# Kernel tuning notes

Measured on AMD Instinct MI355X. Metric: run time of the kernel, lower is better.

Reference implementation:

```python
import jax, jax.numpy as jnp
import numpy as np

B, C, H, W = 4, 192, 128, 128
GAMMA = 0.9
HIDDEN = int(C * 2.66)  # 510
EPS_NORM = 1e-12
EPS_LN = 1e-5


def conv2d(x, w, b, groups=1, pad=0):
    # x: (B,Cin,H,W), w: (Cout, Cin//groups, kh, kw)
    y = jax.lax.conv_general_dilated(
        x, w, window_strides=(1, 1), padding=[(pad, pad), (pad, pad)],
        dimension_numbers=("NCHW", "OIHW", "NCHW"), feature_group_count=groups)
    return y + b[None, :, None, None]


def setup_inputs() -> dict:
    key = jax.random.key(0)
    ks = jax.random.split(key, 32)
    s = 0.02
    d = {
        "Q": jax.random.normal(ks[0], (B, C, H, W), jnp.float32),
        "Fn": jax.random.normal(ks[1], (B, C, H, W), jnp.float32),
        "temperature": jnp.ones((1,), jnp.float32),
        # q/k/v projections: 1x1 conv then depthwise 3x3
        "qw1": jax.random.normal(ks[2], (C, C, 1, 1)) * s, "qb1": jnp.zeros((C,)),
        "qw2": jax.random.normal(ks[3], (C, 1, 3, 3)) * s, "qb2": jnp.zeros((C,)),
        "kw1": jax.random.normal(ks[4], (C, C, 1, 1)) * s, "kb1": jnp.zeros((C,)),
        "kw2": jax.random.normal(ks[5], (C, 1, 3, 3)) * s, "kb2": jnp.zeros((C,)),
        "vw1": jax.random.normal(ks[6], (C, C, 1, 1)) * s, "vb1": jnp.zeros((C,)),
        "vw2": jax.random.normal(ks[7], (C, 1, 3, 3)) * s, "vb2": jnp.zeros((C,)),
        "ow": jax.random.normal(ks[8], (C, C, 1, 1)) * s, "ob": jnp.zeros((C,)),
        # LayerNorm over channels
        "ln_w": jnp.ones((C,)), "ln_b": jnp.zeros((C,)),
        # FFN: proj_in 1x1 -> 2*HIDDEN, dw 3x3 (groups=2*HIDDEN), proj_out HIDDEN -> C
        "fi_w": jax.random.normal(ks[9], (2 * HIDDEN, C, 1, 1)) * s, "fi_b": jnp.zeros((2 * HIDDEN,)),
        "fd_w": jax.random.normal(ks[10], (2 * HIDDEN, 1, 3, 3)) * s, "fd_b": jnp.zeros((2 * HIDDEN,)),
        "fo_w": jax.random.normal(ks[11], (C, HIDDEN, 1, 1)) * s, "fo_b": jnp.zeros((C,)),
    }
    return {k: v.astype(jnp.float32) for k, v in d.items()}


def _forward(Q, Fn, temperature, qw1, qb1, qw2, qb2, kw1, kb1, kw2, kb2,
             vw1, vb1, vw2, vb2, ow, ob, ln_w, ln_b, fi_w, fi_b, fd_w, fd_b, fo_w, fo_b):
    q = conv2d(conv2d(Q, qw1, qb1), qw2, qb2, groups=C, pad=1).reshape(B, C, H * W)
    k = conv2d(conv2d(Fn, kw1, kb1), kw2, kb2, groups=C, pad=1).reshape(B, C, H * W)
    v = conv2d(conv2d(Fn, vw1, vb1), vw2, vb2, groups=C, pad=1).reshape(B, C, H * W)
    # L2 normalize along spatial (last) dim
    q = q / jnp.maximum(jnp.linalg.norm(q, axis=-1, keepdims=True), EPS_NORM)
    k = k / jnp.maximum(jnp.linalg.norm(k, axis=-1, keepdims=True), EPS_NORM)
    attn = jnp.einsum("bcn,bdn->bcd", q, k) * temperature  # (B,C,C)
    attn = jax.nn.softmax(attn, axis=-1)
    k_keep = max(1, int(C * GAMMA))
    topk_vals, _ = jax.lax.top_k(attn, k_keep)
    threshold = topk_vals[:, :, -1:]
    attn = attn * (attn >= threshold).astype(attn.dtype)
    out = jnp.einsum("bcd,bdn->bcn", attn, v).reshape(B, C, H, W)
    Fa = conv2d(out, ow, ob)
    # LayerNorm over channel dim (per pixel)
    xp = Fa.transpose(0, 2, 3, 1)  # (B,H,W,C)
    mu = xp.mean(-1, keepdims=True)
    var = ((xp - mu) ** 2).mean(-1, keepdims=True)
    xn = ((xp - mu) / jnp.sqrt(var + EPS_LN)) * ln_w + ln_b
    xn = xn.transpose(0, 3, 1, 2)
    # FFN
    h = conv2d(xn, fi_w, fi_b)
    h = conv2d(h, fd_w, fd_b, groups=2 * HIDDEN, pad=1)
    x1, x2 = h[:, :HIDDEN], h[:, HIDDEN:]
    h = x1 * jax.nn.gelu(x2, approximate=False)
    ffn_out = conv2d(h, fo_w, fo_b)
    return Fa + ffn_out


def reference(Q, Fn, temperature, qw1, qb1, qw2, qb2, kw1, kb1, kw2, kb2,
              vw1, vb1, vw2, vb2, ow, ob, ln_w, ln_b, fi_w, fi_b, fd_w, fd_b, fo_w, fo_b):
    return _forward(Q, Fn, temperature, qw1, qb1, qw2, qb2, kw1, kb1, kw2, kb2,
                    vw1, vb1, vw2, vb2, ow, ob, ln_w, ln_b, fi_w, fi_b, fd_w, fd_b, fo_w, fo_b)
```

## Files before the change

### kernel.cpp

```cpp
#include <hip/hip_runtime.h>
#include <math.h>
#include <float.h>

#define NPIX 16384
#define CC 192
#define BB 4
#define HHH 128
#define WWW 128
#define HID 510
#define HID2 1020
#define KKEEP 172
#define KSPLIT 16

typedef unsigned short ushort;
typedef unsigned int uint32;
using f32x4  = __attribute__((ext_vector_type(4))) float;
using bf16x8 = __attribute__((ext_vector_type(8))) short;

__device__ __forceinline__ float bf2f(ushort u) {
  union { float f; unsigned int i; } x; x.i = ((unsigned int)u) << 16; return x.f;
}
__device__ __forceinline__ ushort f2bf(float f) {
  union { float f; unsigned int i; } x; x.f = f;
  unsigned int r = (x.i + 0x7FFFu + ((x.i >> 16) & 1u)) >> 16;
// ... 3 lines not shown
struct __align__(16) us8 { ushort u[8]; };
struct __align__(8)  us4 { ushort u[4]; };

__global__ __launch_bounds__(256) void k_wconv(
    const float* __restrict__ fiw, const float* __restrict__ fow,
    ushort* __restrict__ fiwb, ushort* __restrict__ fowb)
{
  const int idx = blockIdx.x * 256 + threadIdx.x;
  if (idx < 1024 * 192) {
    const int r = idx / 192, c = idx % 192;
    fiwb[idx] = (r < HID2) ? f2bf(fiw[r * 192 + c]) : (ushort)0;
  }
  const int i2 = idx - 1024 * 192;
  if (i2 >= 0 && i2 < 192 * 512) {
    const int r = i2 / 512, c = i2 % 512;
    fowb[i2] = (c < HID) ? f2bf(fow[r * HID + c]) : (ushort)0;
  }
}

__global__ __launch_bounds__(256) void k_tsplit(
    const float* __restrict__ X, ushort* __restrict__ Xh, ushort* __restrict__ Xl)
{
  __shared__ float ld[64][261];
  const int b = blockIdx.z;
  const int c0 = blockIdx.y * 64;
  const int px0 = blockIdx.x * 256;
  const int tid = threadIdx.x;
  #pragma unroll
  for (int i = 0; i < 16; ++i) {
    const int u = i * 256 + tid;
    const int r = u >> 6, p4 = (u & 63) * 4;
    const float4 v = *reinterpret_cast<const float4*>(
        X + ((size_t)b * CC + c0 + r) * NPIX + px0 + p4);
    ld[r][p4] = v.x; ld[r][p4 + 1] = v.y; ld[r][p4 + 2] = v.z; ld[r][p4 + 3] = v.w;
  }
  __syncthreads();
  const int c8 = (tid & 7) * 8;
  #pragma unroll
  for (int it = 0; it < 8; ++it) {
    const int pl = it * 32 + (tid >> 3);
    us8 hi, lo;
    #pragma unroll
    for (int j = 0; j < 8; ++j) {
      const float v = ld[c8 + j][pl];
      const ushort h = f2bf(v);
      hi.u[j] = h; lo.u[j] = f2bf(v - bf2f(h));
    }
    const size_t off = ((size_t)b * NPIX + px0 + pl) * CC + c0 + c8;
    *reinterpret_cast<us8*>(Xh + off) = hi;
    *reinterpret_cast<us8*>(Xl + off) = lo;
  }
}

__global__ __launch_bounds__(512) void k_nt3res(
    const float* __restrict__ W,
    const ushort* __restrict__ Bh, const ushort* __restrict__ Bl,
    const float* __restrict__ bias, float* __restrict__ C,
    long long sAb)
{
  __shared__ ushort As[2][64][200];
  __shared__ ushort Bs[2][128][200];
  const int b = blockIdx.z;
  const int n0 = blockIdx.x * 128;
  const int m0 = blockIdx.y * 64;
  const int tid = threadIdx.x;
  const int lane = tid & 63;
  const int wave = tid >> 6;
  const int wm = wave >> 2, wn = wave & 3;
  const float*  Wb  = W  + (size_t)b * sAb;
  const ushort* Bhb = Bh + (size_t)b * NPIX * CC;
  const ushort* Blb = Bl + (size_t)b * NPIX * CC;

  #pragma unroll
  for (int i = 0; i < 6; ++i) {
    const int u = i * 512 + tid;
    const int r = u / 48, c = (u % 48) * 4;
    const float4 v = *reinterpret_cast<const float4*>(Wb + (size_t)(m0 + r) * CC + c);
    const float e[4] = {v.x, v.y, v.z, v.w};
    us4 hi, lo;
    #pragma unroll
    for (int t = 0; t < 4; ++t) {
      const ushort h = f2bf(e[t]);
      hi.u[t] = h; lo.u[t] = f2bf(e[t] - bf2f(h));
    }
    *reinterpret_cast<us4*>(&As[0][r][c]) = hi;
    *reinterpret_cast<us4*>(&As[1][r][c]) = lo;
  }
  #pragma unroll
  for (int i = 0; i < 6; ++i) {
    const int u = i * 512 + tid;
    const int r = u / 24, c = (u % 24) * 8;
    *reinterpret_cast<us8*>(&Bs[0][r][c]) =
        *reinterpret_cast<const us8*>(Bhb + (size_t)(n0 + r) * CC + c);
    *reinterpret_cast<us8*>(&Bs[1][r][c]) =
        *reinterpret_cast<const us8*>(Blb + (size_t)(n0 + r) * CC + c);
  }
  __syncthreads();

  f32x4 acc[2][2];
  #pragma unroll
  for (int i = 0; i < 2; ++i)
    #pragma unroll
    for (int j = 0; j < 2; ++j) acc[i][j] = (f32x4){0.f, 0.f, 0.f, 0.f};

  #pragma unroll
  for (int kk = 0; kk < 6; ++kk) {
    bf16x8 af[2][2], bfg[2][2];
    #pragma unroll
    for (int mi = 0; mi < 2; ++mi)
      #pragma unroll
      for (int p = 0; p < 2; ++p)
        af[mi][p] = *reinterpret_cast<const bf16x8*>(
            &As[p][wm * 32 + mi * 16 + (lane & 15)][kk * 32 + (lane >> 4) * 8]);
    #pragma unroll
    for (int ni = 0; ni < 2; ++ni)
      #pragma unroll
      for (int p = 0; p < 2; ++p)
        bfg[ni][p] = *reinterpret_cast<const bf16x8*>(
            &Bs[p][wn * 32 + ni * 16 + (lane & 15)][kk * 32 + (lane >> 4) * 8]);
    #pragma unroll
    for (int mi = 0; mi < 2; ++mi)
      #pragma unroll
      for (int ni = 0; ni < 2; ++ni) {
        acc[mi][ni] = __builtin_amdgcn_mfma_f32_16x16x32_bf16(
            af[mi][0], bfg[ni][0], acc[mi][ni], 0, 0, 0);
        acc[mi][ni] = __builtin_amdgcn_mfma_f32_16x16x32_bf16(
            af[mi][0], bfg[ni][1], acc[mi][ni], 0, 0, 0);
        acc[mi][ni] = __builtin_amdgcn_mfma_f32_16x16x32_bf16(
            af[mi][1], bfg[ni][0], acc[mi][ni], 0, 0, 0);
      }
  }

  #pragma unroll
  for (int mi = 0; mi < 2; ++mi)
    #pragma unroll
    for (int r = 0; r < 4; ++r) {
      const int m = m0 + wm * 32 + mi * 16 + (lane >> 4) * 4 + r;
      const float bv = bias[m];
      #pragma unroll
      for (int ni = 0; ni < 2; ++ni) {
        const int n = n0 + wn * 32 + ni * 16 + (lane & 15);
        C[(size_t)b * CC * NPIX + (size_t)m * NPIX + n] = acc[mi][ni][r] + bv;
      }
    }
}

__global__ __launch_bounds__(512) void k_nt3res2(
    const float* __restrict__ W1, const float* __restrict__ W2,
    const ushort* __restrict__ Bh, const ushort* __restrict__ Bl,
    const float* __restrict__ b1, const float* __restrict__ b2,
    float* __restrict__ C1, float* __restrict__ C2)
{
  __shared__ ushort As[2][64][200];
  __shared__ ushort Bs[2][128][200];
  const int b = blockIdx.z;
  const int n0 = blockIdx.x * 128;
  const bool sel = blockIdx.y >= 3;
  const int m0 = (sel ? (blockIdx.y - 3) : blockIdx.y) * 64;
  const float* W = sel ? W2 : W1;
  const float* bias = sel ? b2 : b1;
  float* C = sel ? C2 : C1;
  const int tid = threadIdx.x;
  const int lane = tid & 63;
  const int wave = tid >> 6;
  const int wm = wave >> 2, wn = wave & 3;
  const ushort* Bhb = Bh + (size_t)b * NPIX * CC;
  const ushort* Blb = Bl + (size_t)b * NPIX * CC;

  #pragma unroll
  for (int i = 0; i < 6; ++i) {
    const int u = i * 512 + tid;
    const int r = u / 48, c = (u % 48) * 4;
    const float4 v = *reinterpret_cast<const float4*>(W + (size_t)(m0 + r) * CC + c);
    const float e[4] = {v.x, v.y, v.z, v.w};
    us4 hi, lo;
    #pragma unroll
    for (int t = 0; t < 4; ++t) {
      const ushort h = f2bf(e[t]);
      hi.u[t] = h; lo.u[t] = f2bf(e[t] - bf2f(h));
    }
    *reinterpret_cast<us4*>(&As[0][r][c]) = hi;
    *reinterpret_cast<us4*>(&As[1][r][c]) = lo;
  }
  #pragma unroll
  for (int i = 0; i < 6; ++i) {
    const int u = i * 512 + tid;
    const int r = u / 24, c = (u % 24) * 8;
    *reinterpret_cast<us8*>(&Bs[0][r][c]) =
        *reinterpret_cast<const us8*>(Bhb + (size_t)(n0 + r) * CC + c);
    *reinterpret_cast<us8*>(&Bs[1][r][c]) =
        *reinterpret_cast<const us8*>(Blb + (size_t)(n0 + r) * CC + c);
  }
  __syncthreads();

  f32x4 acc[2][2];
  #pragma unroll
  for (int i = 0; i < 2; ++i)
    #pragma unroll
    for (int j = 0; j < 2; ++j) acc[i][j] = (f32x4){0.f, 0.f, 0.f, 0.f};

  #pragma unroll
  for (int kk = 0; kk < 6; ++kk) {
    bf16x8 af[2][2], bfg[2][2];
    #pragma unroll
    for (int mi = 0; mi < 2; ++mi)
      #pragma unroll
      for (int p = 0; p < 2; ++p)
        af[mi][p] = *reinterpret_cast<const bf16x8*>(
            &As[p][wm * 32 + mi * 16 + (lane & 15)][kk * 32 + (lane >> 4) * 8]);
    #pragma unroll
    for (int ni = 0; ni < 2; ++ni)
      #pragma unroll
      for (int p = 0; p < 2; ++p)
        bfg[ni][p] = *reinterpret_cast<const bf16x8*>(
            &Bs[p][wn * 32 + ni * 16 + (lane & 15)][kk * 32 + (lane >> 4) * 8]);
    #pragma unroll
    for (int mi = 0; mi < 2; ++mi)
      #pragma unroll
      for (int ni = 0; ni < 2; ++ni) {
        acc[mi][ni] = __builtin_amdgcn_mfma_f32_16x16x32_bf16(
            af[mi][0], bfg[ni][0], acc[mi][ni], 0, 0, 0);
        acc[mi][ni] = __builtin_amdgcn_mfma_f32_16x16x32_bf16(
            af[mi][0], bfg[ni][1], acc[mi][ni], 0, 0, 0);
        acc[mi][ni] = __builtin_amdgcn_mfma_f32_16x16x32_bf16(
            af[mi][1], bfg[ni][0], acc[mi][ni], 0, 0, 0);
      }
  }

  #pragma unroll
  for (int mi = 0; mi < 2; ++mi)
    #pragma unroll
    for (int r = 0; r < 4; ++r) {
      const int m = m0 + wm * 32 + mi * 16 + (lane >> 4) * 4 + r;
      const float bv = bias[m];
      #pragma unroll
      for (int ni = 0; ni < 2; ++ni) {
        const int n = n0 + wn * 32 + ni * 16 + (lane & 15);
        C[(size_t)b * CC * NPIX + (size_t)m * NPIX + n] = acc[mi][ni][r] + bv;
      }
    }
}

__global__ __launch_bounds__(256) void k_fi(
    const ushort* __restrict__ Aw, const ushort* __restrict__ Bt,
    const float* __restrict__ bias, ushort* __restrict__ H)
{
  __shared__ ushort lds[64 * 200 + 128 * 200];
  ushort (*As)[200] = reinterpret_cast<ushort(*)[200]>(lds);
  ushort (*Bs)[200] = reinterpret_cast<ushort(*)[200]>(lds + 64 * 200);
  ushort (*Cs)[132] = reinterpret_cast<ushort(*)[132]>(lds);
  const int z = blockIdx.z;
  const int n0 = blockIdx.x * 128;
  const int m0 = blockIdx.y * 64;
  const int tid = threadIdx.x;
  const int lane = tid & 63;
  const int wave = tid >> 6;
  const int wm = wave >> 1, wn = wave & 1;
  const ushort* Bb = Bt + (size_t)z * NPIX * CC;
  ushort* Hb = H + (size_t)z * 1024 * NPIX;

  #pragma unroll
  for (int i = 0; i < 6; ++i) {
    const int u = i * 256 + tid;
    const int r = u / 24, c = (u % 24) * 8;
    *reinterpret_cast<us8*>(&As[r][c]) =
        *reinterpret_cast<const us8*>(Aw + (size_t)(m0 + r) * CC + c);
  }
  #pragma unroll
  for (int i = 0; i < 12; ++i) {
    const int u = i * 256 + tid;
    const int r = u / 24, c = (u % 24) * 8;
    *reinterpret_cast<us8*>(&Bs[r][c]) =
        *reinterpret_cast<const us8*>(Bb + (size_t)(n0 + r) * CC + c);
  }
  __syncthreads();

  f32x4 acc[2][4];
  #pragma unroll
  for (int i = 0; i < 2; ++i)
    #pragma unroll
    for (int j = 0; j < 4; ++j) acc[i][j] = (f32x4){0.f, 0.f, 0.f, 0.f};

  #pragma unroll
  for (int kk = 0; kk < 6; ++kk) {
    bf16x8 af[2], bfg[4];
    #pragma unroll
    for (int mi = 0; mi < 2; ++mi)
      af[mi] = *reinterpret_cast<const bf16x8*>(
          &As[wm * 32 + mi * 16 + (lane & 15)][kk * 32 + (lane >> 4) * 8]);
    #pragma unroll
    for (int ni = 0; ni < 4; ++ni)
      bfg[ni] = *reinterpret_cast<const bf16x8*>(
          &Bs[wn * 64 + ni * 16 + (lane & 15)][kk * 32 + (lane >> 4) * 8]);
    #pragma unroll
    for (int mi = 0; mi < 2; ++mi)
      #pragma unroll
      for (int ni = 0; ni < 4; ++ni)
        acc[mi][ni] = __builtin_amdgcn_mfma_f32_16x16x32_bf16(
            af[mi], bfg[ni], acc[mi][ni], 0, 0, 0);
  }

  __syncthreads();
  #pragma unroll
  for (int mi = 0; mi < 2; ++mi)
    #pragma unroll
    for (int rr = 0; rr < 4; ++rr) {
      const int rloc = wm * 32 + mi * 16 + (lane >> 4) * 4 + rr;
      const int m = m0 + rloc;
      const float bv = (m < HID2) ? bias[m] : 0.f;
      #pragma unroll
      for (int ni = 0; ni < 4; ++ni) {
        const int cc = wn * 64 + ni * 16 + (lane & 15);
        Cs[rloc][cc] = f2bf(acc[mi][ni][rr] + bv);
      }
    }
  __syncthreads();
  #pragma unroll
  for (int it = 0; it < 4; ++it) {
    const int r = it * 16 + (tid >> 4);
    const int c8 = (tid & 15) * 8;
    *reinterpret_cast<us8*>(Hb + (size_t)(m0 + r) * NPIX + n0 + c8) =
        *reinterpret_cast<const us8*>(&Cs[r][c8]);
  }
}

__global__ __launch_bounds__(256) void k_fo(
    const ushort* __restrict__ Aw, const ushort* __restrict__ Bt,
    const float* __restrict__ bias, const float* __restrict__ res,
    float* __restrict__ C)
{
  __shared__ ushort As[64][520];
  __shared__ ushort Bs[2][128][136];
  const int z = blockIdx.z;
  const int n0 = blockIdx.x * 128;
  const int m0 = blockIdx.y * 64;
  const int tid = threadIdx.x;
  const int lane = tid & 63;
  const int wave = tid >> 6;
  const int wm = wave >> 1, wn = wave & 1;
  const ushort* Bb = Bt + (size_t)z * NPIX * 512;
  const float* resb = res + (size_t)z * CC * NPIX;
  float* Cb = C + (size_t)z * CC * NPIX;

  #pragma unroll
  for (int i = 0; i < 16; ++i) {
    const int u = i * 256 + tid;
    const int r = u >> 6, c = (u & 63) * 8;
    *reinterpret_cast<us8*>(&As[r][c]) =
        *reinterpret_cast<const us8*>(Aw + (size_t)(m0 + r) * 512 + c);
  }
  #pragma unroll
  for (int i = 0; i < 8; ++i) {
    const int u = i * 256 + tid;
    const int r = u >> 4, c = (u & 15) * 8;
    *reinterpret_cast<us8*>(&Bs[0][r][c]) =
        *reinterpret_cast<const us8*>(Bb + (size_t)(n0 + r) * 512 + c);
  }
  __syncthreads();

  f32x4 acc[2][4];
  #pragma unroll
  for (int i = 0; i < 2; ++i)
    #pragma unroll
    for (int j = 0; j < 4; ++j) acc[i][j] = (f32x4){0.f, 0.f, 0.f, 0.f};

  for (int t = 0; t < 4; ++t) {
    us8 rg[8];
    if (t < 3) {
      #pragma unroll
      for (int i = 0; i < 8; ++i) {
        const int u = i * 256 + tid;
        const int r = u >> 4, c = (u & 15) * 8;
        rg[i] = *reinterpret_cast<const us8*>(
            Bb + (size_t)(n0 + r) * 512 + (t + 1) * 128 + c);
      }
    }
    const int cur = t & 1;
    #pragma unroll
    for (int ks = 0; ks < 4; ++ks) {
      bf16x8 af[2], bfg[4];
      #pragma unroll
      for (int mi = 0; mi < 2; ++mi)
        af[mi] = *reinterpret_cast<const bf16x8*>(
            &As[wm * 32 + mi * 16 + (lane & 15)][t * 128 + ks * 32 + (lane >> 4) * 8]);
      #pragma unroll
      for (int ni = 0; ni < 4; ++ni)
        bfg[ni] = *reinterpret_cast<const bf16x8*>(
            &Bs[cur][wn * 64 + ni * 16 + (lane & 15)][ks * 32 + (lane >> 4) * 8]);
      #pragma unroll
      for (int mi = 0; mi < 2; ++mi)
        #pragma unroll
        for (int ni = 0; ni < 4; ++ni)
          acc[mi][ni] = __builtin_amdgcn_mfma_f32_16x16x32_bf16(
              af[mi], bfg[ni], acc[mi][ni], 0, 0, 0);
    }
    if (t < 3) {
      #pragma unroll
      for (int i = 0; i < 8; ++i) {
        const int u = i * 256 + tid;
        const int r = u >> 4, c = (u & 15) * 8;
        *reinterpret_cast<us8*>(&Bs[cur ^ 1][r][c]) = rg[i];
      }
    }
    __syncthreads();
  }

  #pragma unroll
  for (int mi = 0; mi < 2; ++mi)
    #pragma unroll
    for (int r = 0; r < 4; ++r) {
      const int m = m0 + wm * 32 + mi * 16 + (lane >> 4) * 4 + r;
      const float bv = bias[m];
      #pragma unroll
      for (int ni = 0; ni < 4; ++ni) {
        const int n = n0 + wn * 64 + ni * 16 + (lane & 15);
        Cb[(size_t)m * NPIX + n] = acc[mi][ni][r] + bv + resb[(size_t)m * NPIX + n];
      }
    }
}

__global__ __launch_bounds__(256) void k_attn_mfma(
    const ushort* __restrict__ qh, const ushort* __restrict__ ql,
    const ushort* __restrict__ kh, const ushort* __restrict__ kl,
    float* __restrict__ part)
{
  __shared__ ushort As[2][64][40];
  __shared__ ushort Bs[2][64][40];
  const int b = blockIdx.z;
  const int tr = blockIdx.x / 3, tc = blockIdx.x % 3;
  const int r0 = tr * 64, c0 = tc * 64;
  const int k0 = blockIdx.y * (NPIX / KSPLIT);
  const int tid = threadIdx.x;
  const int lane = tid & 63;
  const int wave = tid >> 6;
  const int wm = wave >> 1, wn = wave & 1;

  f32x4 acc[2][2];
  #pragma unroll
  for (int i = 0; i < 2; ++i)
    #pragma unroll
    for (int j = 0; j < 2; ++j) acc[i][j] = (f32x4){0.f, 0.f, 0.f, 0.f};

  const int ar = tid >> 2, ak = (tid & 3) * 8;

  for (int kc = 0; kc < NPIX / KSPLIT; kc += 32) {
    const size_t qo = (size_t)(b * CC + r0 + ar) * NPIX + k0 + kc + ak;
    const size_t ko = (size_t)(b * CC + c0 + ar) * NPIX + k0 + kc + ak;
// ... 16 lines not shown
        bfr[ni][p] = *reinterpret_cast<const bf16x8*>(
            &Bs[p][wn * 32 + ni * 16 + (lane & 15)][(lane >> 4) * 8]);
    #pragma unroll
    for (int mi = 0; mi < 2; ++mi)
      #pragma unroll
      for (int ni = 0; ni < 2; ++ni) {
        acc[mi][ni] = __builtin_amdgcn_mfma_f32_16x16x32_bf16(
            af[mi][0], bfr[ni][0], acc[mi][ni], 0, 0, 0);
        acc[mi][ni] = __builtin_amdgcn_mfma_f32_16x16x32_bf16(
            af[mi][0], bfr[ni][1], acc[mi][ni], 0, 0, 0);
        acc[mi][ni] = __builtin_amdgcn_mfma_f32_16x16x32_bf16(
            af[mi][1], bfr[ni][0], acc[mi][ni], 0, 0, 0);
      }
    __syncthreads();
  }

  float* pp = part + (size_t)(blockIdx.y * BB + b) * CC * CC;
  #pragma unroll
  for (int mi = 0; mi < 2; ++mi)
    #pragma unroll
    for (int r = 0; r < 4; ++r) {
      const int row = r0 + wm * 32 + mi * 16 + (lane >> 4) * 4 + r;
      #pragma unroll
      for (int ni = 0; ni < 2; ++ni) {
        const int col = c0 + wn * 32 + ni * 16 + (lane & 15);
        pp[(size_t)row * CC + col] = acc[mi][ni][r];
      }
    }
}

__device__ __forceinline__ void dw4(const float* __restrict__ Xc,
                                    const float* __restrict__ wt, float bv,
                                    int h, int w, float out[4])
{
  float a0, a1, a2, a3;
  a0 = a1 = a2 = a3 = bv;
  #pragma unroll
  for (int dy = 0; dy < 3; ++dy) {
    const int hh = h + dy - 1;
    if (hh < 0 || hh >= HHH) continue;
    const float* row = Xc + hh * WWW + w;
    const float xm = (w > 0) ? row[-1] : 0.f;
    const float4 xc = *reinterpret_cast<const float4*>(row);
    const float xp = (w < WWW - 4) ? row[4] : 0.f;
    const float w0 = wt[dy * 3 + 0], w1 = wt[dy * 3 + 1], w2 = wt[dy * 3 + 2];
    a0 += w0 * xm   + w1 * xc.x + w2 * xc.y;
    a1 += w0 * xc.x + w1 * xc.y + w2 * xc.z;
    a2 += w0 * xc.y + w1 * xc.z + w2 * xc.w;
    a3 += w0 * xc.z + w1 * xc.w + w2 * xp;
  }
  out[0] = a0; out[1] = a1; out[2] = a2; out[3] = a3;
}

__global__ __launch_bounds__(256) void k_dw3x3(
    const float* __restrict__ X, const float* __restrict__ W9,
    const float* __restrict__ bias, float* __restrict__ Y)
{
  const int b = blockIdx.z, c = blockIdx.y;
  const int p = blockIdx.x * 1024 + threadIdx.x * 4;
  const int h = p >> 7, w = p & 127;
  float o[4];
  dw4(X + (size_t)(b * CC + c) * NPIX, W9 + c * 9, bias[c], h, w, o);
  *reinterpret_cast<float4*>(Y + (size_t)(b * CC + c) * NPIX + p) =
      make_float4(o[0], o[1], o[2], o[3]);
}

__global__ __launch_bounds__(256) void k_dw3x3_split(
    const float* __restrict__ X, const float* __restrict__ W9,
    const float* __restrict__ bias, ushort* __restrict__ Yh,
    ushort* __restrict__ Yl)
{
  const int b = blockIdx.z, c = blockIdx.y;
  const int p = blockIdx.x * 1024 + threadIdx.x * 4;
  const int h = p >> 7, w = p & 127;
  float o[4];
  dw4(X + (size_t)(b * CC + c) * NPIX, W9 + c * 9, bias[c], h, w, o);
  us4 hi, lo;
  #pragma unroll
  for (int t = 0; t < 4; ++t) {
    const ushort hv = f2bf(o[t]);
    hi.u[t] = hv;
    lo.u[t] = f2bf(o[t] - bf2f(hv));
  }
  const size_t off = (size_t)(b * CC + c) * NPIX + p;
  *reinterpret_cast<us4*>(Yh + off) = hi;
  *reinterpret_cast<us4*>(Yl + off) = lo;
}

__global__ __launch_bounds__(256) void k_rownorm2(
    const ushort* __restrict__ qh, const ushort* __restrict__ ql,
    const ushort* __restrict__ kh, const ushort* __restrict__ kl,
    float* __restrict__ rq, float* __restrict__ rk)
{
  const int row = blockIdx.x;
  const ushort* H = blockIdx.y ? kh : qh;
  const ushort* L = blockIdx.y ? kl : ql;
  float* R = blockIdx.y ? rk : rq;
  const ushort* Hr = H + (size_t)row * NPIX;
  const ushort* Lr = L + (size_t)row * NPIX;
  float s = 0.f;
  for (int i = threadIdx.x * 8; i < NPIX; i += 2048) {
    const us8 a = *reinterpret_cast<const us8*>(Hr + i);
    const us8 bb = *reinterpret_cast<const us8*>(Lr + i);
    #pragma unroll
    for (int t = 0; t < 8; ++t) {
      const float v = bf2f(a.u[t]) + bf2f(bb.u[t]);
      s += v * v;
    }
  }
  __shared__ float sm[256];
  sm[threadIdx.x] = s; __syncthreads();
  for (int st = 128; st > 0; st >>= 1) {
    if (threadIdx.x < st) sm[threadIdx.x] += sm[threadIdx.x + st];
    __syncthreads();
  }
  if (threadIdx.x == 0) R[row] = 1.f / fmaxf(sqrtf(sm[0]), 1e-12f);
}

__global__ __launch_bounds__(192) void k_softmax_topk(
    const float* __restrict__ part, const float* __restrict__ rq,
    const float* __restrict__ rk, const float* __restrict__ temp,
    float* __restrict__ attnm)
{
  const int c = blockIdx.x, b = blockIdx.y, d = threadIdx.x;
  float s = 0.f;
  for (int ksp = 0; ksp < KSPLIT; ++ksp)
    s += part[(size_t)(ksp * BB + b) * CC * CC + c * CC + d];
  const float logit = s * rq[b * CC + c] * rk[b * CC + d] * temp[0];
  __shared__ float sa[CC], sb[CC];
  sa[d] = logit; __syncthreads();
  float mx = -FLT_MAX;
  for (int j = 0; j < CC; ++j) mx = fmaxf(mx, sa[j]);
  const float e = expf(logit - mx);
  sb[d] = e; __syncthreads();
  float sum = 0.f;
  for (int j = 0; j < CC; ++j) sum += sb[j];
  const float pv = e / sum;
  __syncthreads();
  sa[d] = pv; __syncthreads();
  int greater = 0;
  for (int j = 0; j < CC; ++j) greater += (sa[j] > pv) ? 1 : 0;
  const float cand = (greater < KKEEP) ? pv : FLT_MAX;
  sb[d] = cand; __syncthreads();
  float thr = FLT_MAX;
  for (int j = 0; j < CC; ++j) thr = fminf(thr, sb[j]);
  attnm[(size_t)(b * CC + c) * CC + d] = (pv >= thr) ? pv : 0.f;
}

__global__ __launch_bounds__(192) void k_mix(
    const float* __restrict__ ow, const float* __restrict__ attnm,
    float* __restrict__ M)
{
  const int c = blockIdx.x, b = blockIdx.y, d = threadIdx.x;
  float acc = 0.f;
  for (int e = 0; e < CC; ++e)
    acc += ow[c * CC + e] * attnm[(size_t)(b * CC + e) * CC + d];
  M[(size_t)(b * CC + c) * CC + d] = acc;
}

__global__ __launch_bounds__(256) void k_ln_t(
    const float* __restrict__ X, const float* __restrict__ lw,
    const float* __restrict__ lb, ushort* __restrict__ Y)
{
  const int b = blockIdx.y;
  const int n = blockIdx.x * 256 + threadIdx.x;
  const float* Xb = X + (size_t)b * CC * NPIX + n;
  float s = 0.f, s2 = 0.f;
  for (int ci = 0; ci < CC; ++ci) {
    const float v = Xb[(size_t)ci * NPIX];
// ... 104 lines not shown
    gsd[j * 129 + (px_l >> 1) + 1] = p1;
  }
  __syncthreads();

  const ushort* gsu = (const ushort*)gsd;
  const int px_l2 = tid;
  const int px = (h0 + (px_l2 >> 7)) * WWW + (px_l2 & 127);
  us8 v;
  #pragma unroll
  for (int t = 0; t < 8; ++t) v.u[t] = gsu[t * 258 + px_l2];
  *reinterpret_cast<us8*>(gt + ((size_t)z * NPIX + px) * 512 + c0) = v;
}

extern "C" void kernel_launch(void* const* d_in, const int* in_sizes, int n_in,
                              void* d_out, int out_size, void* d_ws, size_t ws_size,
                              hipStream_t stream)
{
  const float* Q    = (const float*)d_in[0];
  const float* Fn   = (const float*)d_in[1];
  const float* temp = (const float*)d_in[2];
  const float* qw1  = (const float*)d_in[3];
  const float* qb1  = (const float*)d_in[4];
  const float* qw2  = (const float*)d_in[5];
  const float* qb2  = (const float*)d_in[6];
  const float* kw1  = (const float*)d_in[7];
  const float* kb1  = (const float*)d_in[8];
  const float* kw2  = (const float*)d_in[9];
  const float* kb2  = (const float*)d_in[10];
  const float* vw1  = (const float*)d_in[11];
  const float* vb1  = (const float*)d_in[12];
  const float* vw2  = (const float*)d_in[13];
  const float* vb2  = (const float*)d_in[14];
  const float* ow   = (const float*)d_in[15];
  const float* ob   = (const float*)d_in[16];
  const float* lnw  = (const float*)d_in[17];
  const float* lnb  = (const float*)d_in[18];
  const float* fiw  = (const float*)d_in[19];
  const float* fib  = (const float*)d_in[20];
  const float* fdw  = (const float*)d_in[21];
  const float* fdb  = (const float*)d_in[22];
  const float* fow  = (const float*)d_in[23];
  const float* fob  = (const float*)d_in[24];
  float* out = (float*)d_out;

  char* ws = (char*)d_ws;
  const size_t P = 25165824UL;
  ushort* Qth = (ushort*)(ws + 0 * P);
  ushort* Qtl = (ushort*)(ws + 1 * P);
  ushort* Fth = (ushort*)(ws + 2 * P);
  ushort* Ftl = (ushort*)(ws + 3 * P);
  ushort* qh  = (ushort*)(ws + 4 * P);
  ushort* ql  = (ushort*)(ws + 5 * P);
  float*  vtmp = (float*)(ws + 0 * P);
  float*  vbuf = (float*)(ws + 2 * P);
  ushort* kh  = (ushort*)(ws + 0 * P);
  ushort* kl  = (ushort*)(ws + 1 * P);
  ushort* vth = (ushort*)(ws + 0 * P);
  ushort* vtl = (ushort*)(ws + 1 * P);
  char* smb = ws + 6 * P;
  float* rq    = (float*)(smb);
  float* rk    = (float*)(smb + 4096);
  float* part  = (float*)(smb + 8192);
  float* attnm = (float*)(smb + 8192 + 9437184);
  float* Mm    = (float*)(smb + 8192 + 9437184 + 589824);
  float*  Fa   = (float*)(ws + 4 * P);
  ushort* xnt  = (ushort*)(ws + 0 * P);
  ushort* h2   = (ushort*)(ws + 1 * P);
  ushort* gt2  = (ushort*)(ws + 6 * P);
  ushort* fiwb = (ushort*)(ws + 6 * P + 33554432UL);
  ushort* fowb = (ushort*)(ws + 6 * P + 33554432UL + 393216UL);
  float* bufT = out;

  dim3 blk(256);
  dim3 blk512(512);

  k_wconv<<<dim3(1152), blk, 0, stream>>>(fiw, fow, fiwb, fowb);
  k_tsplit<<<dim3(64, 3, BB), blk, 0, stream>>>(Q,  Qth, Qtl);
  k_tsplit<<<dim3(64, 3, BB), blk, 0, stream>>>(Fn, Fth, Ftl);
  k_nt3res<<<dim3(128, 3, BB), blk512, 0, stream>>>(qw1, Qth, Qtl, qb1, bufT, 0);
  k_dw3x3_split<<<dim3(16, CC, BB), blk, 0, stream>>>(bufT, qw2, qb2, qh, ql);
  k_nt3res2<<<dim3(128, 6, BB), blk512, 0, stream>>>(kw1, vw1, Fth, Ftl,
                                                     kb1, vb1, bufT, vtmp);
  k_dw3x3<<<dim3(16, CC, BB), blk, 0, stream>>>(vtmp, vw2, vb2, vbuf);
  k_dw3x3_split<<<dim3(16, CC, BB), blk, 0, stream>>>(bufT, kw2, kb2, kh, kl);
  k_rownorm2<<<dim3(BB * CC, 2), blk, 0, stream>>>(qh, ql, kh, kl, rq, rk);
  k_attn_mfma<<<dim3(9, KSPLIT, BB), blk, 0, stream>>>(qh, ql, kh, kl, part);
  k_softmax_topk<<<dim3(CC, BB), dim3(192), 0, stream>>>(part, rq, rk, temp, attnm);
  k_mix<<<dim3(CC, BB), dim3(192), 0, stream>>>(ow, attnm, Mm);
  k_tsplit<<<dim3(64, 3, BB), blk, 0, stream>>>(vbuf, vth, vtl);
  k_nt3res<<<dim3(128, 3, BB), blk512, 0, stream>>>(Mm, vth, vtl, ob, Fa,
                                                    (long long)CC * CC);
  k_ln_t<<<dim3(64, BB), blk, 0, stream>>>(Fa, lnw, lnb, xnt);
  for (int p = 0; p < 2; ++p) {
    const ushort* xn_p = xnt + (size_t)(2 * p) * NPIX * CC;
    const float*  fa_p = Fa + (size_t)(2 * p) * CC * NPIX;
    float* out_p = out + (size_t)(2 * p) * CC * NPIX;
    k_fi<<<dim3(128, 16, 2), blk, 0, stream>>>(fiwb, xn_p, fib, h2);
    k_dwglu3<<<dim3(64, 64, 2), blk, 0, stream>>>(h2, fdw, fdb, gt2);
    k_fo<<<dim3(128, 3, 2), blk, 0, stream>>>(fowb, gt2, fob, fa_p, out_p);
  }
}
```

Baseline: 628.3 us.

## Hold GEMM weight fragments in registers and stage hi/lo B halves sequentially

The 1x1-conv GEMM kernels now load weight (A) fragments straight from global memory into registers, with the bf16 hi/lo split done in registers, instead of staging them in LDS. The 3-term kernels also stage the B hi and lo halves one after the other through a single LDS buffer. This cuts LDS use per block, which should allow more blocks per CU, and removes LDS reads for A. In exchange it adds register pressure, an extra barrier phase, and uncoalesced per-lane weight loads.

```diff
diff --git a/kernel.cpp b/kernel.cpp
--- a/kernel.cpp
+++ b/kernel.cpp
@@ -79,14 +79,13 @@
   }
 }
 
-__global__ __launch_bounds__(512) void k_nt3res(
+__global__ __launch_bounds__(512) void k_nt3reg(
     const float* __restrict__ W,
     const ushort* __restrict__ Bh, const ushort* __restrict__ Bl,
     const float* __restrict__ bias, float* __restrict__ C,
     long long sAb)
 {
-  __shared__ ushort As[2][64][200];
-  __shared__ ushort Bs[2][128][200];
+  __shared__ ushort Bs[128][200];
   const int b = blockIdx.z;
   const int n0 = blockIdx.x * 128;
   const int m0 = blockIdx.y * 64;
@@ -98,64 +97,80 @@
   const ushort* Bhb = Bh + (size_t)b * NPIX * CC;
   const ushort* Blb = Bl + (size_t)b * NPIX * CC;
 
-  #pragma unroll
-  for (int i = 0; i < 6; ++i) {
-    const int u = i * 512 + tid;
-    const int r = u / 48, c = (u % 48) * 4;
-    const float4 v = *reinterpret_cast<const float4*>(Wb + (size_t)(m0 + r) * CC + c);
-    const float e[4] = {v.x, v.y, v.z, v.w};
-    us4 hi, lo;
-    #pragma unroll
-    for (int t = 0; t < 4; ++t) {
-      const ushort h = f2bf(e[t]);
-      hi.u[t] = h; lo.u[t] = f2bf(e[t] - bf2f(h));
-    }
-    *reinterpret_cast<us4*>(&As[0][r][c]) = hi;
-    *reinterpret_cast<us4*>(&As[1][r][c]) = lo;
-  }
+  bf16x8 ah[2][6], al[2][6];
+  #pragma unroll
+  for (int mi = 0; mi < 2; ++mi) {
+    const int row = m0 + wm * 32 + mi * 16 + (lane & 15);
+    #pragma unroll
+    for (int kk = 0; kk < 6; ++kk) {
+      const int col = kk * 32 + (lane >> 4) * 8;
+      const float4 v0 = *reinterpret_cast<const float4*>(Wb + (size_t)row * CC + col);
+      const float4 v1 = *reinterpret_cast<const float4*>(Wb + (size_t)row * CC + col + 4);
+      const float e[8] = {v0.x, v0.y, v0.z, v0.w, v1.x, v1.y, v1.z, v1.w};
+      bf16x8 h8, l8;
+      #pragma unroll
+      for (int t = 0; t < 8; ++t) {
+        const ushort h = f2bf(e[t]);
+        h8[t] = (short)h;
+        l8[t] = (short)f2bf(e[t] - bf2f(h));
+      }
+      ah[mi][kk] = h8; al[mi][kk] = l8;
+    }
+  }
+
+  f32x4 acc[2][2];
+  #pragma unroll
+  for (int i = 0; i < 2; ++i)
+    #pragma unroll
+    for (int j = 0; j < 2; ++j) acc[i][j] = (f32x4){0.f, 0.f, 0.f, 0.f};
+
   #pragma unroll
   for (int i = 0; i < 6; ++i) {
     const int u = i * 512 + tid;
     const int r = u / 24, c = (u % 24) * 8;
-    *reinterpret_cast<us8*>(&Bs[0][r][c]) =
+    *reinterpret_cast<us8*>(&Bs[r][c]) =
         *reinterpret_cast<const us8*>(Bhb + (size_t)(n0 + r) * CC + c);
-    *reinterpret_cast<us8*>(&Bs[1][r][c]) =
+  }
+  __syncthreads();
+  #pragma unroll
+  for (int kk = 0; kk < 6; ++kk) {
+    bf16x8 bfg[2];
+    #pragma unroll
+    for (int ni = 0; ni < 2; ++ni)
+      bfg[ni] = *reinterpret_cast<const bf16x8*>(
+          &Bs[wn * 32 + ni * 16 + (lane & 15)][kk * 32 + (lane >> 4) * 8]);
+    #pragma unroll
+    for (int mi = 0; mi < 2; ++mi)
+      #pragma unroll
+      for (int ni = 0; ni < 2; ++ni) {
+        acc[mi][ni] = __builtin_amdgcn_mfma_f32_16x16x32_bf16(
+            ah[mi][kk], bfg[ni], acc[mi][ni], 0, 0, 0);
+        acc[mi][ni] = __builtin_amdgcn_mfma_f32_16x16x32_bf16(
+            al[mi][kk], bfg[ni], acc[mi][ni], 0, 0, 0);
+      }
+  }
+  __syncthreads();
+  #pragma unroll
+  for (int i = 0; i < 6; ++i) {
+    const int u = i * 512 + tid;
+    const int r = u / 24, c = (u % 24) * 8;
+    *reinterpret_cast<us8*>(&Bs[r][c]) =
         *reinterpret_cast<const us8*>(Blb + (size_t)(n0 + r) * CC + c);
   }
   __syncthreads();
-
-  f32x4 acc[2][2];
-  #pragma unroll
-  for (int i = 0; i < 2; ++i)
-    #pragma unroll
-    for (int j = 0; j < 2; ++j) acc[i][j] = (f32x4){0.f, 0.f, 0.f, 0.f};
-
   #pragma unroll
   for (int kk = 0; kk < 6; ++kk) {
-    bf16x8 af[2][2], bfg[2][2];
+    bf16x8 bfg[2];
+    #pragma unroll
+    for (int ni = 0; ni < 2; ++ni)
+      bfg[ni] = *reinterpret_cast<const bf16x8*>(
+          &Bs[wn * 32 + ni * 16 + (lane & 15)][kk * 32 + (lane >> 4) * 8]);
     #pragma unroll
     for (int mi = 0; mi < 2; ++mi)
       #pragma unroll
-      for (int p = 0; p < 2; ++p)
-        af[mi][p] = *reinterpret_cast<const bf16x8*>(
-            &As[p][wm * 32 + mi * 16 + (lane & 15)][kk * 32 + (lane >> 4) * 8]);
-    #pragma unroll
-    for (int ni = 0; ni < 2; ++ni)
-      #pragma unroll
-      for (int p = 0; p < 2; ++p)
-        bfg[ni][p] = *reinterpret_cast<const bf16x8*>(
-            &Bs[p][wn * 32 + ni * 16 + (lane & 15)][kk * 32 + (lane >> 4) * 8]);
-    #pragma unroll
-    for (int mi = 0; mi < 2; ++mi)
-      #pragma unroll
-      for (int ni = 0; ni < 2; ++ni) {
-        acc[mi][ni] = __builtin_amdgcn_mfma_f32_16x16x32_bf16(
-            af[mi][0], bfg[ni][0], acc[mi][ni], 0, 0, 0);
-        acc[mi][ni] = __builtin_amdgcn_mfma_f32_16x16x32_bf16(
-            af[mi][0], bfg[ni][1], acc[mi][ni], 0, 0, 0);
-        acc[mi][ni] = __builtin_amdgcn_mfma_f32_16x16x32_bf16(
-            af[mi][1], bfg[ni][0], acc[mi][ni], 0, 0, 0);
-      }
+      for (int ni = 0; ni < 2; ++ni)
+        acc[mi][ni] = __builtin_amdgcn_mfma_f32_16x16x32_bf16(
+            ah[mi][kk], bfg[ni], acc[mi][ni], 0, 0, 0);
   }
 
   #pragma unroll
@@ -172,14 +187,13 @@
     }
 }
 
-__global__ __launch_bounds__(512) void k_nt3res2(
+__global__ __launch_bounds__(512) void k_nt3reg2(
     const float* __restrict__ W1, const float* __restrict__ W2,
     const ushort* __restrict__ Bh, const ushort* __restrict__ Bl,
     const float* __restrict__ b1, const float* __restrict__ b2,
     float* __restrict__ C1, float* __restrict__ C2)
 {
-  __shared__ ushort As[2][64][200];
-  __shared__ ushort Bs[2][128][200];
+  __shared__ ushort Bs[128][200];
   const int b = blockIdx.z;
   const int n0 = blockIdx.x * 128;
   const bool sel = blockIdx.y >= 3;
@@ -194,64 +208,80 @@
   const ushort* Bhb = Bh + (size_t)b * NPIX * CC;
   const ushort* Blb = Bl + (size_t)b * NPIX * CC;
 
-  #pragma unroll
-  for (int i = 0; i < 6; ++i) {
-    const int u = i * 512 + tid;
-    const int r = u / 48, c = (u % 48) * 4;
-    const float4 v = *reinterpret_cast<const float4*>(W + (size_t)(m0 + r) * CC + c);
-    const float e[4] = {v.x, v.y, v.z, v.w};
-    us4 hi, lo;
-    #pragma unroll
-    for (int t = 0; t < 4; ++t) {
-      const ushort h = f2bf(e[t]);
-      hi.u[t] = h; lo.u[t] = f2bf(e[t] - bf2f(h));
-    }
-    *reinterpret_cast<us4*>(&As[0][r][c]) = hi;
-    *reinterpret_cast<us4*>(&As[1][r][c]) = lo;
-  }
+  bf16x8 ah[2][6], al[2][6];
+  #pragma unroll
+  for (int mi = 0; mi < 2; ++mi) {
+    const int row = m0 + wm * 32 + mi * 16 + (lane & 15);
+    #pragma unroll
+    for (int kk = 0; kk < 6; ++kk) {
+      const int col = kk * 32 + (lane >> 4) * 8;
+      const float4 v0 = *reinterpret_cast<const float4*>(W + (size_t)row * CC + col);
+      const float4 v1 = *reinterpret_cast<const float4*>(W + (size_t)row * CC + col + 4);
+      const float e[8] = {v0.x, v0.y, v0.z, v0.w, v1.x, v1.y, v1.z, v1.w};
+      bf16x8 h8, l8;
+      #pragma unroll
+      for (int t = 0; t < 8; ++t) {
+        const ushort h = f2bf(e[t]);
+        h8[t] = (short)h;
+        l8[t] = (short)f2bf(e[t] - bf2f(h));
+      }
+      ah[mi][kk] = h8; al[mi][kk] = l8;
+    }
+  }
+
+  f32x4 acc[2][2];
+  #pragma unroll
+  for (int i = 0; i < 2; ++i)
+    #pragma unroll
+    for (int j = 0; j < 2; ++j) acc[i][j] = (f32x4){0.f, 0.f, 0.f, 0.f};
+
   #pragma unroll
   for (int i = 0; i < 6; ++i) {
     const int u = i * 512 + tid;
     const int r = u / 24, c = (u % 24) * 8;
-    *reinterpret_cast<us8*>(&Bs[0][r][c]) =
+    *reinterpret_cast<us8*>(&Bs[r][c]) =
         *reinterpret_cast<const us8*>(Bhb + (size_t)(n0 + r) * CC + c);
-    *reinterpret_cast<us8*>(&Bs[1][r][c]) =
+  }
+  __syncthreads();
+  #pragma unroll
+  for (int kk = 0; kk < 6; ++kk) {
+    bf16x8 bfg[2];
+    #pragma unroll
+    for (int ni = 0; ni < 2; ++ni)
+      bfg[ni] = *reinterpret_cast<const bf16x8*>(
+          &Bs[wn * 32 + ni * 16 + (lane & 15)][kk * 32 + (lane >> 4) * 8]);
+    #pragma unroll
+    for (int mi = 0; mi < 2; ++mi)
+      #pragma unroll
+      for (int ni = 0; ni < 2; ++ni) {
+        acc[mi][ni] = __builtin_amdgcn_mfma_f32_16x16x32_bf16(
+            ah[mi][kk], bfg[ni], acc[mi][ni], 0, 0, 0);
+        acc[mi][ni] = __builtin_amdgcn_mfma_f32_16x16x32_bf16(
+            al[mi][kk], bfg[ni], acc[mi][ni], 0, 0, 0);
+      }
+  }
+  __syncthreads();
+  #pragma unroll
+  for (int i = 0; i < 6; ++i) {
+    const int u = i * 512 + tid;
+    const int r = u / 24, c = (u % 24) * 8;
+    *reinterpret_cast<us8*>(&Bs[r][c]) =
         *reinterpret_cast<const us8*>(Blb + (size_t)(n0 + r) * CC + c);
   }
   __syncthreads();
-
-  f32x4 acc[2][2];
-  #pragma unroll
-  for (int i = 0; i < 2; ++i)
-    #pragma unroll
-    for (int j = 0; j < 2; ++j) acc[i][j] = (f32x4){0.f, 0.f, 0.f, 0.f};
-
   #pragma unroll
   for (int kk = 0; kk < 6; ++kk) {
-    bf16x8 af[2][2], bfg[2][2];
+    bf16x8 bfg[2];
+    #pragma unroll
+    for (int ni = 0; ni < 2; ++ni)
+      bfg[ni] = *reinterpret_cast<const bf16x8*>(
+          &Bs[wn * 32 + ni * 16 + (lane & 15)][kk * 32 + (lane >> 4) * 8]);
     #pragma unroll
     for (int mi = 0; mi < 2; ++mi)
       #pragma unroll
-      for (int p = 0; p < 2; ++p)
-        af[mi][p] = *reinterpret_cast<const bf16x8*>(
-            &As[p][wm * 32 + mi * 16 + (lane & 15)][kk * 32 + (lane >> 4) * 8]);
-    #pragma unroll
-    for (int ni = 0; ni < 2; ++ni)
-      #pragma unroll
-      for (int p = 0; p < 2; ++p)
-        bfg[ni][p] = *reinterpret_cast<const bf16x8*>(
-            &Bs[p][wn * 32 + ni * 16 + (lane & 15)][kk * 32 + (lane >> 4) * 8]);
-    #pragma unroll
-    for (int mi = 0; mi < 2; ++mi)
-      #pragma unroll
-      for (int ni = 0; ni < 2; ++ni) {
-        acc[mi][ni] = __builtin_amdgcn_mfma_f32_16x16x32_bf16(
-            af[mi][0], bfg[ni][0], acc[mi][ni], 0, 0, 0);
-        acc[mi][ni] = __builtin_amdgcn_mfma_f32_16x16x32_bf16(
-            af[mi][0], bfg[ni][1], acc[mi][ni], 0, 0, 0);
-        acc[mi][ni] = __builtin_amdgcn_mfma_f32_16x16x32_bf16(
-            af[mi][1], bfg[ni][0], acc[mi][ni], 0, 0, 0);
-      }
+      for (int ni = 0; ni < 2; ++ni)
+        acc[mi][ni] = __builtin_amdgcn_mfma_f32_16x16x32_bf16(
+            ah[mi][kk], bfg[ni], acc[mi][ni], 0, 0, 0);
   }
 
   #pragma unroll
@@ -272,10 +302,8 @@
     const ushort* __restrict__ Aw, const ushort* __restrict__ Bt,
     const float* __restrict__ bias, ushort* __restrict__ H)
 {
-  __shared__ ushort lds[64 * 200 + 128 * 200];
-  ushort (*As)[200] = reinterpret_cast<ushort(*)[200]>(lds);
-  ushort (*Bs)[200] = reinterpret_cast<ushort(*)[200]>(lds + 64 * 200);
-  ushort (*Cs)[132] = reinterpret_cast<ushort(*)[132]>(lds);
+  __shared__ ushort Bs[128][200];
+  ushort (*Cs)[132] = reinterpret_cast<ushort(*)[132]>(&Bs[0][0]);
   const int z = blockIdx.z;
   const int n0 = blockIdx.x * 128;
   const int m0 = blockIdx.y * 64;
@@ -286,13 +314,16 @@
   const ushort* Bb = Bt + (size_t)z * NPIX * CC;
   ushort* Hb = H + (size_t)z * 1024 * NPIX;
 
-  #pragma unroll
-  for (int i = 0; i < 6; ++i) {
-    const int u = i * 256 + tid;
-    const int r = u / 24, c = (u % 24) * 8;
-    *reinterpret_cast<us8*>(&As[r][c]) =
-        *reinterpret_cast<const us8*>(Aw + (size_t)(m0 + r) * CC + c);
-  }
+  bf16x8 ah[2][6];
+  #pragma unroll
+  for (int mi = 0; mi < 2; ++mi) {
+    const int row = m0 + wm * 32 + mi * 16 + (lane & 15);
+    #pragma unroll
+    for (int kk = 0; kk < 6; ++kk)
+      ah[mi][kk] = *reinterpret_cast<const bf16x8*>(
+          Aw + (size_t)row * CC + kk * 32 + (lane >> 4) * 8);
+  }
+
   #pragma unroll
   for (int i = 0; i < 12; ++i) {
     const int u = i * 256 + tid;
@@ -310,11 +341,7 @@
 
   #pragma unroll
   for (int kk = 0; kk < 6; ++kk) {
-    bf16x8 af[2], bfg[4];
-    #pragma unroll
-    for (int mi = 0; mi < 2; ++mi)
-      af[mi] = *reinterpret_cast<const bf16x8*>(
-          &As[wm * 32 + mi * 16 + (lane & 15)][kk * 32 + (lane >> 4) * 8]);
+    bf16x8 bfg[4];
     #pragma unroll
     for (int ni = 0; ni < 4; ++ni)
       bfg[ni] = *reinterpret_cast<const bf16x8*>(
@@ -324,7 +351,7 @@
       #pragma unroll
       for (int ni = 0; ni < 4; ++ni)
         acc[mi][ni] = __builtin_amdgcn_mfma_f32_16x16x32_bf16(
-            af[mi], bfg[ni], acc[mi][ni], 0, 0, 0);
+            ah[mi][kk], bfg[ni], acc[mi][ni], 0, 0, 0);
   }
 
   __syncthreads();
@@ -356,7 +383,6 @@
     const float* __restrict__ bias, const float* __restrict__ res,
     float* __restrict__ C)
 {
-  __shared__ ushort As[64][520];
   __shared__ ushort Bs[2][128][136];
   const int z = blockIdx.z;
   const int n0 = blockIdx.x * 128;
@@ -369,13 +395,16 @@
   const float* resb = res + (size_t)z * CC * NPIX;
   float* Cb = C + (size_t)z * CC * NPIX;
 
-  #pragma unroll
-  for (int i = 0; i < 16; ++i) {
-    const int u = i * 256 + tid;
-    const int r = u >> 6, c = (u & 63) * 8;
-    *reinterpret_cast<us8*>(&As[r][c]) =
-        *reinterpret_cast<const us8*>(Aw + (size_t)(m0 + r) * 512 + c);
-  }
+  bf16x8 ah[2][16];
+  #pragma unroll
+  for (int mi = 0; mi < 2; ++mi) {
+    const int row = m0 + wm * 32 + mi * 16 + (lane & 15);
+    #pragma unroll
+    for (int ks = 0; ks < 16; ++ks)
+      ah[mi][ks] = *reinterpret_cast<const bf16x8*>(
+          Aw + (size_t)row * 512 + ks * 32 + (lane >> 4) * 8);
+  }
+
   #pragma unroll
   for (int i = 0; i < 8; ++i) {
     const int u = i * 256 + tid;
@@ -405,11 +434,7 @@
     const int cur = t & 1;
     #pragma unroll
     for (int ks = 0; ks < 4; ++ks) {
-      bf16x8 af[2], bfg[4];
-      #pragma unroll
-      for (int mi = 0; mi < 2; ++mi)
-        af[mi] = *reinterpret_cast<const bf16x8*>(
-            &As[wm * 32 + mi * 16 + (lane & 15)][t * 128 + ks * 32 + (lane >> 4) * 8]);
+      bf16x8 bfg[4];
       #pragma unroll
       for (int ni = 0; ni < 4; ++ni)
         bfg[ni] = *reinterpret_cast<const bf16x8*>(
@@ -419,7 +444,7 @@
         #pragma unroll
         for (int ni = 0; ni < 4; ++ni)
           acc[mi][ni] = __builtin_amdgcn_mfma_f32_16x16x32_bf16(
-              af[mi], bfg[ni], acc[mi][ni], 0, 0, 0);
+              ah[mi][t * 4 + ks], bfg[ni], acc[mi][ni], 0, 0, 0);
     }
     if (t < 3) {
       #pragma unroll
@@ -840,9 +865,9 @@
   k_wconv<<<dim3(1152), blk, 0, stream>>>(fiw, fow, fiwb, fowb);
   k_tsplit<<<dim3(64, 3, BB), blk, 0, stream>>>(Q,  Qth, Qtl);
   k_tsplit<<<dim3(64, 3, BB), blk, 0, stream>>>(Fn, Fth, Ftl);
-  k_nt3res<<<dim3(128, 3, BB), blk512, 0, stream>>>(qw1, Qth, Qtl, qb1, bufT, 0);
+  k_nt3reg<<<dim3(128, 3, BB), blk512, 0, stream>>>(qw1, Qth, Qtl, qb1, bufT, 0);
   k_dw3x3_split<<<dim3(16, CC, BB), blk, 0, stream>>>(bufT, qw2, qb2, qh, ql);
-  k_nt3res2<<<dim3(128, 6, BB), blk512, 0, stream>>>(kw1, vw1, Fth, Ftl,
+  k_nt3reg2<<<dim3(128, 6, BB), blk512, 0, stream>>>(kw1, vw1, Fth, Ftl,
                                                      kb1, vb1, bufT, vtmp);
   k_dw3x3<<<dim3(16, CC, BB), blk, 0, stream>>>(vtmp, vw2, vb2, vbuf);
   k_dw3x3_split<<<dim3(16, CC, BB), blk, 0, stream>>>(bufT, kw2, kb2, kh, kl);
@@ -851,7 +876,7 @@
   k_softmax_topk<<<dim3(CC, BB), dim3(192), 0, stream>>>(part, rq, rk, temp, attnm);
   k_mix<<<dim3(CC, BB), dim3(192), 0, stream>>>(ow, attnm, Mm);
   k_tsplit<<<dim3(64, 3, BB), blk, 0, stream>>>(vbuf, vth, vtl);
-  k_nt3res<<<dim3(128, 3, BB), blk512, 0, stream>>>(Mm, vth, vtl, ob, Fa,
+  k_nt3reg<<<dim3(128, 3, BB), blk512, 0, stream>>>(Mm, vth, vtl, ob, Fa,
                                                     (long long)CC * CC);
   k_ln_t<<<dim3(64, BB), blk, 0, stream>>>(Fa, lnw, lnb, xnt);
   for (int p = 0; p < 2; ++p) {
```

New measurement: 748.3 us. 19.1% more time.

## Fuse row-norm partials into depthwise conv and transpose-split V in dwconv

Applied to the files above, without the earlier changes.

The q/k depthwise-conv split kernels now also compute per-block sums of squares into a partials buffer, and a tiny finalize kernel turns those into inverse norms. This replaces the separate row-norm kernel that re-read the full q/k hi/lo tensors. The V depthwise conv is rewritten to stage results in shared memory and write the transposed bf16 hi/lo split directly, which removes the fp32 intermediate and the separate transpose-split pass. The norm now sums the fp32 values before the hi/lo split rather than the reconstructed hi+lo values, a small numerical difference. Buffer aliasing is reorganised so V's split tensors live in slots 2 and 3.

```diff
diff --git a/kernel.cpp b/kernel.cpp
--- a/kernel.cpp
+++ b/kernel.cpp
@@ -542,23 +542,10 @@
   out[0] = a0; out[1] = a1; out[2] = a2; out[3] = a3;
 }
 
-__global__ __launch_bounds__(256) void k_dw3x3(
-    const float* __restrict__ X, const float* __restrict__ W9,
-    const float* __restrict__ bias, float* __restrict__ Y)
-{
-  const int b = blockIdx.z, c = blockIdx.y;
-  const int p = blockIdx.x * 1024 + threadIdx.x * 4;
-  const int h = p >> 7, w = p & 127;
-  float o[4];
-  dw4(X + (size_t)(b * CC + c) * NPIX, W9 + c * 9, bias[c], h, w, o);
-  *reinterpret_cast<float4*>(Y + (size_t)(b * CC + c) * NPIX + p) =
-      make_float4(o[0], o[1], o[2], o[3]);
-}
-
 __global__ __launch_bounds__(256) void k_dw3x3_split(
     const float* __restrict__ X, const float* __restrict__ W9,
     const float* __restrict__ bias, ushort* __restrict__ Yh,
-    ushort* __restrict__ Yl)
+    ushort* __restrict__ Yl, float* __restrict__ partial)
 {
   const int b = blockIdx.z, c = blockIdx.y;
   const int p = blockIdx.x * 1024 + threadIdx.x * 4;
@@ -575,36 +562,70 @@
   const size_t off = (size_t)(b * CC + c) * NPIX + p;
   *reinterpret_cast<us4*>(Yh + off) = hi;
   *reinterpret_cast<us4*>(Yl + off) = lo;
-}
-
-__global__ __launch_bounds__(256) void k_rownorm2(
-    const ushort* __restrict__ qh, const ushort* __restrict__ ql,
-    const ushort* __restrict__ kh, const ushort* __restrict__ kl,
-    float* __restrict__ rq, float* __restrict__ rk)
-{
-  const int row = blockIdx.x;
-  const ushort* H = blockIdx.y ? kh : qh;
-  const ushort* L = blockIdx.y ? kl : ql;
-  float* R = blockIdx.y ? rk : rq;
-  const ushort* Hr = H + (size_t)row * NPIX;
-  const ushort* Lr = L + (size_t)row * NPIX;
-  float s = 0.f;
-  for (int i = threadIdx.x * 8; i < NPIX; i += 2048) {
-    const us8 a = *reinterpret_cast<const us8*>(Hr + i);
-    const us8 bb = *reinterpret_cast<const us8*>(Lr + i);
-    #pragma unroll
-    for (int t = 0; t < 8; ++t) {
-      const float v = bf2f(a.u[t]) + bf2f(bb.u[t]);
-      s += v * v;
-    }
-  }
   __shared__ float sm[256];
-  sm[threadIdx.x] = s; __syncthreads();
+  sm[threadIdx.x] = o[0]*o[0] + o[1]*o[1] + o[2]*o[2] + o[3]*o[3];
+  __syncthreads();
   for (int st = 128; st > 0; st >>= 1) {
     if (threadIdx.x < st) sm[threadIdx.x] += sm[threadIdx.x + st];
     __syncthreads();
   }
-  if (threadIdx.x == 0) R[row] = 1.f / fmaxf(sqrtf(sm[0]), 1e-12f);
+  if (threadIdx.x == 0)
+    partial[(size_t)(b * CC + c) * 16 + blockIdx.x] = sm[0];
+}
+
+__global__ __launch_bounds__(256) void k_rnfin(
+    const float* __restrict__ pq, const float* __restrict__ pk,
+    float* __restrict__ rq, float* __restrict__ rk)
+{
+  const int row = blockIdx.x * 256 + threadIdx.x;
+  if (row >= BB * CC) return;
+  const float* p = blockIdx.y ? pk : pq;
+  float s = 0.f;
+  for (int i = 0; i < 16; ++i) s += p[(size_t)row * 16 + i];
+  (blockIdx.y ? rk : rq)[row] = 1.f / fmaxf(sqrtf(s), 1e-12f);
+}
+
+__global__ __launch_bounds__(256) void k_dw3x3t(
+    const float* __restrict__ X, const float* __restrict__ W9,
+    const float* __restrict__ bias, ushort* __restrict__ Yh,
+    ushort* __restrict__ Yl)
+{
+  __shared__ float ld[64][68];
+  const int b = blockIdx.z;
+  const int c0 = blockIdx.y * 64;
+  const int p0 = blockIdx.x * 64;
+  const int h = p0 >> 7;
+  const int w0 = p0 & 127;
+  const int tid = threadIdx.x;
+  const int ch = tid >> 2;
+  const float* Xc = X + (size_t)(b * CC + c0 + ch) * NPIX;
+  const float* wt = W9 + (size_t)(c0 + ch) * 9;
+  const float bv = bias[c0 + ch];
+  #pragma unroll
+  for (int i = 0; i < 4; ++i) {
+    const int q = (tid & 3) + 4 * i;
+    const int w = w0 + q * 4;
+    float o[4];
+    dw4(Xc, wt, bv, h, w, o);
+    ld[ch][q * 4 + 0] = o[0]; ld[ch][q * 4 + 1] = o[1];
+    ld[ch][q * 4 + 2] = o[2]; ld[ch][q * 4 + 3] = o[3];
+  }
+  __syncthreads();
+  const int c8 = (tid & 7) * 8;
+  #pragma unroll
+  for (int it = 0; it < 2; ++it) {
+    const int pl = it * 32 + (tid >> 3);
+    us8 hi, lo;
+    #pragma unroll
+    for (int j = 0; j < 8; ++j) {
+      const float v = ld[c8 + j][pl];
+      const ushort hv = f2bf(v);
+      hi.u[j] = hv; lo.u[j] = f2bf(v - bf2f(hv));
+    }
+    const size_t off = ((size_t)b * NPIX + p0 + pl) * CC + c0 + c8;
+    *reinterpret_cast<us8*>(Yh + off) = hi;
+    *reinterpret_cast<us8*>(Yl + off) = lo;
+  }
 }
 
 __global__ __launch_bounds__(192) void k_softmax_topk(
@@ -815,17 +836,18 @@
   ushort* qh  = (ushort*)(ws + 4 * P);
   ushort* ql  = (ushort*)(ws + 5 * P);
   float*  vtmp = (float*)(ws + 0 * P);
-  float*  vbuf = (float*)(ws + 2 * P);
+  ushort* vth = (ushort*)(ws + 2 * P);
+  ushort* vtl = (ushort*)(ws + 3 * P);
   ushort* kh  = (ushort*)(ws + 0 * P);
   ushort* kl  = (ushort*)(ws + 1 * P);
-  ushort* vth = (ushort*)(ws + 0 * P);
-  ushort* vtl = (ushort*)(ws + 1 * P);
   char* smb = ws + 6 * P;
   float* rq    = (float*)(smb);
   float* rk    = (float*)(smb + 4096);
   float* part  = (float*)(smb + 8192);
   float* attnm = (float*)(smb + 8192 + 9437184);
   float* Mm    = (float*)(smb + 8192 + 9437184 + 589824);
+  float* pq    = (float*)(smb + 8192 + 9437184 + 2 * 589824);
+  float* pk    = (float*)(smb + 8192 + 9437184 + 2 * 589824 + 49152);
   float*  Fa   = (float*)(ws + 4 * P);
   ushort* xnt  = (ushort*)(ws + 0 * P);
   ushort* h2   = (ushort*)(ws + 1 * P);
@@ -841,16 +863,15 @@
   k_tsplit<<<dim3(64, 3, BB), blk, 0, stream>>>(Q,  Qth, Qtl);
   k_tsplit<<<dim3(64, 3, BB), blk, 0, stream>>>(Fn, Fth, Ftl);
   k_nt3res<<<dim3(128, 3, BB), blk512, 0, stream>>>(qw1, Qth, Qtl, qb1, bufT, 0);
-  k_dw3x3_split<<<dim3(16, CC, BB), blk, 0, stream>>>(bufT, qw2, qb2, qh, ql);
+  k_dw3x3_split<<<dim3(16, CC, BB), blk, 0, stream>>>(bufT, qw2, qb2, qh, ql, pq);
   k_nt3res2<<<dim3(128, 6, BB), blk512, 0, stream>>>(kw1, vw1, Fth, Ftl,
                                                      kb1, vb1, bufT, vtmp);
-  k_dw3x3<<<dim3(16, CC, BB), blk, 0, stream>>>(vtmp, vw2, vb2, vbuf);
-  k_dw3x3_split<<<dim3(16, CC, BB), blk, 0, stream>>>(bufT, kw2, kb2, kh, kl);
-  k_rownorm2<<<dim3(BB * CC, 2), blk, 0, stream>>>(qh, ql, kh, kl, rq, rk);
+  k_dw3x3t<<<dim3(256, 3, BB), blk, 0, stream>>>(vtmp, vw2, vb2, vth, vtl);
+  k_dw3x3_split<<<dim3(16, CC, BB), blk, 0, stream>>>(bufT, kw2, kb2, kh, kl, pk);
+  k_rnfin<<<dim3(3, 2), blk, 0, stream>>>(pq, pk, rq, rk);
   k_attn_mfma<<<dim3(9, KSPLIT, BB), blk, 0, stream>>>(qh, ql, kh, kl, part);
   k_softmax_topk<<<dim3(CC, BB), dim3(192), 0, stream>>>(part, rq, rk, temp, attnm);
   k_mix<<<dim3(CC, BB), dim3(192), 0, stream>>>(ow, attnm, Mm);
-  k_tsplit<<<dim3(64, 3, BB), blk, 0, stream>>>(vbuf, vth, vtl);
   k_nt3res<<<dim3(128, 3, BB), blk512, 0, stream>>>(Mm, vth, vtl, ob, Fa,
                                                     (long long)CC * CC);
   k_ln_t<<<dim3(64, BB), blk, 0, stream>>>(Fa, lnw, lnb, xnt);
```

New measurement: 650.2 us. 1.03x slower.
